# Optimization experiments

Measured on AMD Instinct MI355X. Metric: run time of the kernel, lower is better.

Reference implementation:

```python
import jax, jax.numpy as jnp
import numpy as np

N_NODES = 100000
N_EDGES = 3200000
NFEAT, NHID, NCLASS = 512, 256, 64


def spmm(rows, cols, vals, x):
    # out[i] = sum_{e: rows[e]==i} vals[e] * x[cols[e]]
    msgs = vals[:, None] * x[cols]  # [E, F]
    return jax.ops.segment_sum(msgs, rows, num_segments=N_NODES)


def setup_inputs() -> dict:
    key = jax.random.key(0)
    ks = jax.random.split(key, 12)
    x = jax.random.normal(ks[0], (N_NODES, NFEAT), dtype=jnp.float32)
    adj_rows = jax.random.randint(ks[1], (N_EDGES,), 0, N_NODES, dtype=jnp.int32)
    adj_cols = jax.random.randint(ks[2], (N_EDGES,), 0, N_NODES, dtype=jnp.int32)
    adj_vals = jax.random.uniform(ks[3], (N_EDGES,), dtype=jnp.float32)
    # xavier-uniform style init for linear weights
    def xavier(k, fan_in, fan_out):
        a = np.sqrt(6.0 / (fan_in + fan_out)).astype(np.float32)
        return jax.random.uniform(k, (fan_in, fan_out), minval=-a, maxval=a, dtype=jnp.float32)
    W1 = xavier(ks[4], NFEAT, NHID)
    b1 = jnp.zeros((NHID,), dtype=jnp.float32)
    W2 = xavier(ks[5], NHID, NCLASS)
    b2 = jnp.zeros((NCLASS,), dtype=jnp.float32)
    Wres = xavier(ks[6], NHID, NCLASS)
    bres = jnp.zeros((NCLASS,), dtype=jnp.float32)
    return {"x": x, "adj_rows": adj_rows, "adj_cols": adj_cols, "adj_vals": adj_vals,
            "W1": W1, "b1": b1, "W2": W2, "b2": b2, "Wres": Wres, "bres": bres}


def reference(x, adj_rows, adj_cols, adj_vals, W1, b1, W2, b2, Wres, bres):
    # layer 1: spmm -> linear (res_con True but last_hidden is None -> no residual)
    h = spmm(adj_rows, adj_cols, adj_vals, x)          # [N, NFEAT]
    h = h @ W1 + b1                                    # [N, NHID]
    last_hidden = h
    # dropout in eval mode: identity
    # layer 2: spmm -> linear -> relu + res(last_hidden) since NHID != NCLASS
    o = spmm(adj_rows, adj_cols, adj_vals, h)          # [N, NHID]
    o = o @ W2 + b2                                    # [N, NCLASS]
    o = jax.nn.relu(o) + (last_hidden @ Wres + bres)   # [N, NCLASS]
    return o
```

## Files before the change

### kernel.cpp

```cpp
#include <hip/hip_runtime.h>

#define N_NODES 100000
#define N_EDGES 3200000
#define NFEAT 512
#define NHID 256
#define NCLASS 64
#define FCAT 128

#define RPB 32
#define NB 3125
#define CHUNK 16384
#define NCH 196

#define ISC14 (1.0f / 16384.0f)
#define ISC10 (1.0f / 1024.0f)

typedef __attribute__((ext_vector_type(8))) short short8;
typedef __attribute__((ext_vector_type(4))) float f32x4;

static __device__ __forceinline__ unsigned short f2bf(float f) {
    unsigned u = __float_as_uint(f);
    unsigned r = (u + 0x7FFF + ((u >> 16) & 1)) >> 16;
    return (unsigned short)r;
}
static __device__ __forceinline__ short8 cvt8(float4 x, float4 y) {
    short8 r;
    r[0] = (short)f2bf(x.x); r[1] = (short)f2bf(x.y);
    r[2] = (short)f2bf(x.z); r[3] = (short)f2bf(x.w);
    r[4] = (short)f2bf(y.x); r[5] = (short)f2bf(y.y);
    r[6] = (short)f2bf(y.z); r[7] = (short)f2bf(y.w);
    return r;
}
__device__ __forceinline__ void gload_lds16(const unsigned short* g, unsigned short* l) {
    __builtin_amdgcn_global_load_lds(
        (const __attribute__((address_space(1))) unsigned int*)g,
        (__attribute__((address_space(3))) unsigned int*)l, 16, 0, 0);
}
static __device__ __forceinline__ int f2q4(float a) {
    return __float2int_rn(fminf(fmaxf(a, -7.9375f), 7.9375f) * 16.f);
}

__global__ __launch_bounds__(256) void k_fusedA(const float* __restrict__ W1,
                                                const float* __restrict__ W2,
                                                const float* __restrict__ Wres,
                                                const float* __restrict__ b1,
                                                const float* __restrict__ bres,
                                                unsigned short* __restrict__ WT,
                                                float* __restrict__ c2,
                                                float* __restrict__ cr,
                                                const int* __restrict__ rows,
                                                int* __restrict__ HT) {
    __shared__ int h[NB];
    int tid = threadIdx.x;
    if (blockIdx.x < 256) {
        int k = blockIdx.x * 2 + (tid >> 7);
        int j = tid & 127;
        const float* wb = (j < NCLASS) ? W2 : Wres;
        int jj = j & (NCLASS - 1);
        const float* w1row = W1 + (size_t)k * NHID;
        float acc = 0.f;
        for (int m = 0; m < NHID; ++m)
            acc += w1row[m] * wb[(size_t)m * NCLASS + jj];
        WT[(size_t)j * NFEAT + k] = f2bf(acc);
        return;
    }
    if (blockIdx.x == 256) {
        if (tid < 128) {
            int j = tid;
            const float* wb = (j < NCLASS) ? W2 : Wres;
            int jj = j & (NCLASS - 1);
            float acc = 0.f;
            for (int m = 0; m < NHID; ++m)
                acc += b1[m] * wb[(size_t)m * NCLASS + jj];
            if (j < NCLASS) c2[jj] = acc;
            else            cr[jj] = acc + bres[jj];
        }
        return;
    }
    int c = blockIdx.x - 257;
    for (int i = tid; i < NB; i += 256) h[i] = 0;
    __syncthreads();
    int e0 = c * CHUNK;
    int eend = e0 + CHUNK; if (eend > N_EDGES) eend = N_EDGES;
    int i = e0 + tid;
    for (; i + 7 * 256 < eend; i += 8 * 256) {
        int r[8];
#pragma unroll
        for (int u = 0; u < 8; ++u) r[u] = rows[i + u * 256];
#pragma unroll
        for (int u = 0; u < 8; ++u) atomicAdd(&h[r[u] >> 5], 1);
    }
    for (; i < eend; i += 256)
        atomicAdd(&h[rows[i] >> 5], 1);
    __syncthreads();
    for (int k = tid; k < NB; k += 256)
        HT[(size_t)k * NCH + c] = h[k];
}

__global__ void k_scan_chunks(const int* __restrict__ HT, int* __restrict__ OFS,
                              int* __restrict__ T) {
    int b = blockIdx.x;
    int lane = threadIdx.x;
    const int* hb = HT + (size_t)b * NCH;
    int run = 0;
    for (int c0 = 0; c0 < NCH; c0 += 64) {
        int idx = c0 + lane;
        int v = (idx < NCH) ? hb[idx] : 0;
        int inc = v;
#pragma unroll
        for (int d = 1; d < 64; d <<= 1) {
            int t = __shfl_up(inc, d);
            if (lane >= d) inc += t;
        }
        if (idx < NCH) OFS[(size_t)idx * NB + b] = run + inc - v;
        run += __shfl(inc, 63);
    }
    if (lane == 0) T[b] = run;
}

__global__ void k_scan_base(const int* __restrict__ T, int* __restrict__ base) {
    int lane = threadIdx.x;
    int run = 0;
    for (int c0 = 0; c0 < NB; c0 += 64) {
        int idx = c0 + lane;
        int v = (idx < NB) ? T[idx] : 0;
        int inc = v;
#pragma unroll
        for (int d = 1; d < 64; d <<= 1) {
            int t = __shfl_up(inc, d);
            if (lane >= d) inc += t;
        }
        if (idx < NB) base[idx] = run + inc - v;
        run += __shfl(inc, 63);
    }
    if (lane == 0) base[NB] = run;
}

__global__ __launch_bounds__(256) void k_partition(const int* __restrict__ rows,
                                                   const int* __restrict__ cols,
                                                   const float* __restrict__ vals,
                                                   const int* __restrict__ OFS,
                                                   const int* __restrict__ base,
                                                   unsigned* __restrict__ stage) {
    __shared__ int cur[NB];
    int c = blockIdx.x;
    int tid = threadIdx.x;
    for (int i = tid; i < NB; i += 256)
        cur[i] = base[i] + OFS[(size_t)c * NB + i];
    __syncthreads();
    int e0 = c * CHUNK;
    int eend = e0 + CHUNK; if (eend > N_EDGES) eend = N_EDGES;
    int i = e0 + tid;
    for (; i + 7 * 256 < eend; i += 8 * 256) {
        int r[8], cc[8]; float v[8];
#pragma unroll
        for (int u = 0; u < 8; ++u) r[u] = rows[i + u * 256];
#pragma unroll
        for (int u = 0; u < 8; ++u) cc[u] = cols[i + u * 256];
#pragma unroll
        for (int u = 0; u < 8; ++u) v[u] = vals[i + u * 256];
        int p[8];
#pragma unroll
        for (int u = 0; u < 8; ++u) p[u] = atomicAdd(&cur[r[u] >> 5], 1);
#pragma unroll
        for (int u = 0; u < 8; ++u) {
            unsigned v10 = min(1023u, (unsigned)__float2int_rn(v[u] * 1024.f));
            stage[p[u]] = (((unsigned)(r[u] & 31)) << 27) |
                          (((unsigned)cc[u]) << 10) | v10;
        }
    }
    for (; i < eend; i += 256) {
        int r = rows[i];
        int p = atomicAdd(&cur[r >> 5], 1);
        unsigned v10 = min(1023u, (unsigned)__float2int_rn(vals[i] * 1024.f));
        stage[p] = (((unsigned)(r & 31)) << 27) | (((unsigned)cols[i]) << 10) | v10;
    }
}

#define GBK 64
__global__ __launch_bounds__(256) void k_gemm_a(const float* __restrict__ X,
                                                const unsigned short* __restrict__ WT,
                                                unsigned short* __restrict__ A2) {
    __shared__ __align__(16) unsigned short Bs[2][FCAT * GBK];
    int tid = threadIdx.x;
    int lane = tid & 63, w = tid >> 6;
    int lr = lane & 15, ls = lane >> 4;
    int row = blockIdx.x * 64 + w * 16 + lr;
    if (row >= N_NODES) row = N_NODES - 1;
    const float* pA = X + (size_t)row * NFEAT;

#define STAGE(buf, k0)                                                         \
    {                                                                          \
        _Pragma("unroll")                                                      \
        for (int q = 0; q < 4; ++q) {                                          \
            int sidx = q * 256 + tid;                                          \
            int n = sidx >> 3, c8 = sidx & 7;                                  \
            const unsigned short* src =                                        \
                WT + (size_t)n * NFEAT + (k0) + ((c8 ^ (n & 7)) << 3);         \
            unsigned short* dst = &Bs[buf][(size_t)(q * 256 + w * 64) * 8];    \
            gload_lds16(src, dst);                                             \
        }                                                                      \
    }

    f32x4 acc[8] = {};
    STAGE(0, 0);
    float4 a00 = *(const float4*)(pA + ls * 8);
    float4 a01 = *(const float4*)(pA + ls * 8 + 4);
    float4 a10 = *(const float4*)(pA + 32 + ls * 8);
    float4 a11 = *(const float4*)(pA + 32 + ls * 8 + 4);
    __syncthreads();
    int cur = 0;

#pragma unroll
    for (int t = 0; t < 8; ++t) {
        float4 n00, n01, n10, n11;
        if (t < 7) {
            const int k1 = (t + 1) * GBK;
            n00 = *(const float4*)(pA + k1 + ls * 8);
            n01 = *(const float4*)(pA + k1 + ls * 8 + 4);
            n10 = *(const float4*)(pA + k1 + 32 + ls * 8);
            n11 = *(const float4*)(pA + k1 + 32 + ls * 8 + 4);
            STAGE(cur ^ 1, k1);
        }

        short8 af0 = cvt8(a00, a01);
        short8 af1 = cvt8(a10, a11);
        const unsigned short* bb = &Bs[cur][0];
#pragma unroll
        for (int nf = 0; nf < 8; ++nf) {
            int n = nf * 16 + lr;
            int p0 = ls ^ (n & 7);
            int p1 = (4 + ls) ^ (n & 7);
            short8 b0 = *(const short8*)(bb + (size_t)n * 64 + p0 * 8);
            short8 b1 = *(const short8*)(bb + (size_t)n * 64 + p1 * 8);
            acc[nf] = __builtin_amdgcn_mfma_f32_16x16x32_bf16(af0, b0, acc[nf], 0, 0, 0);
            acc[nf] = __builtin_amdgcn_mfma_f32_16x16x32_bf16(af1, b1, acc[nf], 0, 0, 0);
        }
        __syncthreads();
        cur ^= 1;
        a00 = n00; a01 = n01; a10 = n10; a11 = n11;
    }
#undef STAGE

#pragma unroll
    for (int j = 0; j < 4; ++j) {
        int gr = blockIdx.x * 64 + w * 16 + ls * 4 + j;
        if (gr < N_NODES) {
#pragma unroll
            for (int nf = 0; nf < 4; ++nf) {
                int il = f2q4(acc[nf][j]);
                int ih = f2q4(acc[nf + 4][j]);
                A2[(size_t)gr * 64 + nf * 16 + lr] =
                    (unsigned short)(((unsigned)il & 0xffu) | (((unsigned)ih & 0xffu) << 8));
            }
        }
    }
}

__global__ __launch_bounds__(256) void k_spmm1(const unsigned short* __restrict__ A2,
                                               const int* __restrict__ base,
                                               const unsigned* __restrict__ stage,
                                               unsigned short* __restrict__ S1a,
                                               float* __restrict__ S1r) {
    __shared__ int acc[RPB][FCAT];
    int b = blockIdx.x, tid = threadIdx.x;
    int wv = tid >> 6, lane = tid & 63;
    unsigned lane2 = (unsigned)lane << 1;
    int4* az = (int4*)&acc[0][0];
    for (int i = tid; i < RPB * FCAT / 4; i += 256) az[i] = make_int4(0, 0, 0, 0);
    __syncthreads();

    const char* A2b = (const char*)A2;

    int s = base[b], e = base[b + 1];
    int per = (e - s + 3) >> 2;
    int ws = s + wv * per;
    int we = ws + per; if (we > e) we = e;
    int t = ws;
    for (; t + 16 <= we; t += 16) {
        unsigned cv[16];
#pragma unroll
        for (int u = 0; u < 16; ++u) cv[u] = stage[t + u];
        unsigned short p[16];
#pragma unroll
        for (int u = 0; u < 16; ++u)
            p[u] = *(const unsigned short*)(A2b + (((cv[u] & 0x07FFFC00u) >> 3) | lane2));
#pragma unroll
        for (int u = 0; u < 16; ++u) {
            int v10 = (int)(cv[u] & 0x3FFu);
            int alo = (int)(signed char)(p[u] & 0xffu);
            int ahi = (int)(signed char)(p[u] >> 8);
            int rl = (int)(cv[u] >> 27);
            atomicAdd(&acc[rl][lane],      __mul24(alo, v10));
            atomicAdd(&acc[rl][lane + 64], __mul24(ahi, v10));
        }
    }
    for (; t < we; ++t) {
        unsigned cv = stage[t];
        unsigned short p = *(const unsigned short*)(A2b + (((cv & 0x07FFFC00u) >> 3) | lane2));
        int v10 = (int)(cv & 0x3FFu);
        int alo = (int)(signed char)(p & 0xffu);
        int ahi = (int)(signed char)(p >> 8);
        int rl = (int)(cv >> 27);
        atomicAdd(&acc[rl][lane],      __mul24(alo, v10));
        atomicAdd(&acc[rl][lane + 64], __mul24(ahi, v10));
    }
    __syncthreads();

#pragma unroll
    for (int rr = 0; rr < 8; ++rr) {
        int r = wv * 8 + rr;
        int node = b * RPB + r;
        int sf = (acc[r][lane] + 32) >> 6;
        sf = max(-32760, min(32760, sf));
        S1a[(size_t)node * 64 + (lane & 31) * 2 + (lane >> 5)] = (unsigned short)sf;
        S1r[(size_t)node * 64 + lane] = (float)acc[r][lane + 64] * ISC14;
    }
}

__global__ __launch_bounds__(256) void k_spmm2_out(const unsigned* __restrict__ S1aP,
                                                   const float* __restrict__ S1r,
                                                   const int* __restrict__ base,
                                                   const unsigned* __restrict__ stage,
                                                   const float* __restrict__ c2,
                                                   const float* __restrict__ cr,
                                                   const float* __restrict__ b2,
                                                   float* __restrict__ out) {
    __shared__ int acc[RPB][NCLASS];
    __shared__ int rs[RPB];
    int b = blockIdx.x, tid = threadIdx.x;
    int wv = tid >> 6, lane = tid & 63;
    int h = lane >> 5, l5 = lane & 31;
    unsigned l54 = (unsigned)l5 << 2;
    int4* az = (int4*)&acc[0][0];
    for (int i = tid; i < RPB * NCLASS / 4; i += 256) az[i] = make_int4(0, 0, 0, 0);
    if (tid < RPB) rs[tid] = 0;
    __syncthreads();

    const char* Sb = (const char*)S1aP;

    int s = base[b], e = base[b + 1];
    int per = (e - s + 3) >> 2;
    int ws = s + wv * per;
    int we = ws + per; if (we > e) we = e;
    int t = ws;
    for (; t + 32 <= we; t += 32) {
        unsigned cv[16];
#pragma unroll
        for (int u = 0; u < 16; ++u) cv[u] = stage[t + u * 2 + h];
        unsigned p[16];
#pragma unroll
        for (int u = 0; u < 16; ++u)
            p[u] = *(const unsigned*)(Sb + (((cv[u] & 0x07FFFC00u) >> 3) | l54));
#pragma unroll
        for (int u = 0; u < 16; ++u) {
            int v10 = (int)(cv[u] & 0x3FFu);
            int slo = (int)(short)(p[u] & 0xffffu);
            int shi = (int)p[u] >> 16;
            int rl = (int)(cv[u] >> 27);
            atomicAdd(&acc[rl][l5],      (__mul24(slo, v10) + 8) >> 4);
            atomicAdd(&acc[rl][l5 + 32], (__mul24(shi, v10) + 8) >> 4);
            if (l5 == 0) atomicAdd(&rs[rl], v10);
        }
    }
    for (; t < we; t += 2) {
        int idx = t + h;
        bool act = idx < we;
        unsigned cv = stage[act ? idx : t];
        unsigned p = *(const unsigned*)(Sb + (((cv & 0x07FFFC00u) >> 3) | l54));
        int v10 = (int)(cv & 0x3FFu);
        int slo = (int)(short)(p & 0xffffu);
        int shi = (int)p >> 16;
        int rl = (int)(cv >> 27);
        if (act) {
            atomicAdd(&acc[rl][l5],      (__mul24(slo, v10) + 8) >> 4);
            atomicAdd(&acc[rl][l5 + 32], (__mul24(shi, v10) + 8) >> 4);
            if (l5 == 0) atomicAdd(&rs[rl], v10);
        }
    }
    __syncthreads();

#pragma unroll
    for (int rr = 0; rr < 8; ++rr) {
        int r = wv * 8 + rr;
        int node = b * RPB + r;
        float facc = (float)acc[r][lane] * ISC14;
        float rsum = (float)rs[r] * ISC10;
        float o = facc + rsum * c2[lane] + b2[lane];
        float res = S1r[(size_t)node * 64 + lane] + cr[lane];
        out[(size_t)node * 64 + lane] = fmaxf(o, 0.f) + res;
    }
}

extern "C" void kernel_launch(void* const* d_in, const int* in_sizes, int n_in,
                              void* d_out, int out_size, void* d_ws, size_t ws_size,
                              hipStream_t stream) {
    const float* x        = (const float*)d_in[0];
    const int*   adj_rows = (const int*)d_in[1];
    const int*   adj_cols = (const int*)d_in[2];
    const float* adj_vals = (const float*)d_in[3];
    const float* W1       = (const float*)d_in[4];
    const float* b1       = (const float*)d_in[5];
    const float* W2       = (const float*)d_in[6];
    const float* b2       = (const float*)d_in[7];
    const float* Wres     = (const float*)d_in[8];
    const float* bres     = (const float*)d_in[9];
    float* out = (float*)d_out;

    char* ws = (char*)d_ws;
    size_t off = 0;
    auto alloc = [&](size_t bytes) {
        size_t o = off;
        off += (bytes + 511) & ~511ULL;
        return o;
    };

    unsigned short* WT  = (unsigned short*)(ws + alloc((size_t)NFEAT * FCAT * 2));
    float* c2           = (float*)(ws + alloc(NCLASS * 4));
    float* cr           = (float*)(ws + alloc(NCLASS * 4));
    unsigned* stage     = (unsigned*)(ws + alloc((size_t)N_EDGES * 4));
    unsigned short* A2  = (unsigned short*)(ws + alloc((size_t)N_NODES * 64 * 2));
    unsigned* S1a       = (unsigned*)(ws + alloc((size_t)N_NODES * 32 * 4));
    char* s1r_region    = ws + alloc((size_t)N_NODES * 64 * 4);
    float* S1r          = (float*)s1r_region;
    int*   HT           = (int*)s1r_region;
    int*   OFS          = (int*)(s1r_region + (((size_t)NB * NCH * 4 + 511) & ~511ULL));
    int*   T            = (int*)(ws + alloc((size_t)NB * 4));
    int*   base         = (int*)(ws + alloc((size_t)(NB + 1) * 4));
    (void)ws_size; (void)in_sizes; (void)n_in; (void)out_size;

    k_fusedA<<<257 + NCH, 256, 0, stream>>>(W1, W2, Wres, b1, bres, WT, c2, cr,
                                            adj_rows, HT);

    k_scan_chunks<<<NB, 64, 0, stream>>>(HT, OFS, T);
    k_scan_base<<<1, 64, 0, stream>>>(T, base);

    k_partition<<<NCH, 256, 0, stream>>>(adj_rows, adj_cols, adj_vals, OFS, base, stage);

    k_gemm_a<<<(N_NODES + 63) / 64, 256, 0, stream>>>(x, WT, A2);

    k_spmm1<<<NB, 256, 0, stream>>>(A2, base, stage, (unsigned short*)S1a, S1r);

    k_spmm2_out<<<NB, 256, 0, stream>>>(S1a, S1r, base, stage, c2, cr, b2, out);
}
```

Measured before the change: 310.3 us.

## Bucket edges by column tile within row blocks to improve gather locality

The counting-sort partition now keys each edge on both its row block and its column range, using four column tiles of 32768 nodes. Each SpMM block then walks the tiles in turn, so gathers from the feature arrays stay inside a narrower address window at any moment and should hit L2 more often. In exchange the histogram and offset tables become four times larger, the chunk count drops to 49 so the partition kernels have fewer blocks, and k_scan_base serially scans 12500 keys in a single wave. There are also more short segments per block, which adds loop overhead.

```diff
diff --git a/kernel.cpp b/kernel.cpp
--- a/kernel.cpp
+++ b/kernel.cpp
@@ -9,8 +9,10 @@
 
 #define RPB 32
 #define NB 3125
-#define CHUNK 16384
-#define NCH 196
+#define NCT 4
+#define NKEY (NCT * NB)
+#define CHUNK 65536
+#define NCH 49
 
 #define ISC14 (1.0f / 16384.0f)
 #define ISC10 (1.0f / 1024.0f)
@@ -49,8 +51,9 @@
                                                 float* __restrict__ c2,
                                                 float* __restrict__ cr,
                                                 const int* __restrict__ rows,
+                                                const int* __restrict__ cols,
                                                 int* __restrict__ HT) {
-    __shared__ int h[NB];
+    __shared__ int h[NKEY];
     int tid = threadIdx.x;
     if (blockIdx.x < 256) {
         int k = blockIdx.x * 2 + (tid >> 7);
@@ -78,22 +81,25 @@
         return;
     }
     int c = blockIdx.x - 257;
-    for (int i = tid; i < NB; i += 256) h[i] = 0;
+    for (int i = tid; i < NKEY; i += 256) h[i] = 0;
     __syncthreads();
     int e0 = c * CHUNK;
     int eend = e0 + CHUNK; if (eend > N_EDGES) eend = N_EDGES;
     int i = e0 + tid;
     for (; i + 7 * 256 < eend; i += 8 * 256) {
-        int r[8];
+        int r[8], cc[8];
 #pragma unroll
         for (int u = 0; u < 8; ++u) r[u] = rows[i + u * 256];
 #pragma unroll
-        for (int u = 0; u < 8; ++u) atomicAdd(&h[r[u] >> 5], 1);
+        for (int u = 0; u < 8; ++u) cc[u] = cols[i + u * 256];
+#pragma unroll
+        for (int u = 0; u < 8; ++u)
+            atomicAdd(&h[(cc[u] >> 15) * NB + (r[u] >> 5)], 1);
     }
     for (; i < eend; i += 256)
-        atomicAdd(&h[rows[i] >> 5], 1);
-    __syncthreads();
-    for (int k = tid; k < NB; k += 256)
+        atomicAdd(&h[(cols[i] >> 15) * NB + (rows[i] >> 5)], 1);
+    __syncthreads();
+    for (int k = tid; k < NKEY; k += 256)
         HT[(size_t)k * NCH + c] = h[k];
 }
 
@@ -112,41 +118,41 @@
             int t = __shfl_up(inc, d);
             if (lane >= d) inc += t;
         }
-        if (idx < NCH) OFS[(size_t)idx * NB + b] = run + inc - v;
+        if (idx < NCH) OFS[(size_t)idx * NKEY + b] = run + inc - v;
         run += __shfl(inc, 63);
     }
     if (lane == 0) T[b] = run;
 }
 
-__global__ void k_scan_base(const int* __restrict__ T, int* __restrict__ base) {
+__global__ void k_scan_base(const int* __restrict__ T, int* __restrict__ base2) {
     int lane = threadIdx.x;
     int run = 0;
-    for (int c0 = 0; c0 < NB; c0 += 64) {
+    for (int c0 = 0; c0 < NKEY; c0 += 64) {
         int idx = c0 + lane;
-        int v = (idx < NB) ? T[idx] : 0;
+        int v = (idx < NKEY) ? T[idx] : 0;
         int inc = v;
 #pragma unroll
         for (int d = 1; d < 64; d <<= 1) {
             int t = __shfl_up(inc, d);
             if (lane >= d) inc += t;
         }
-        if (idx < NB) base[idx] = run + inc - v;
+        if (idx < NKEY) base2[idx] = run + inc - v;
         run += __shfl(inc, 63);
     }
-    if (lane == 0) base[NB] = run;
+    if (lane == 0) base2[NKEY] = run;
 }
 
 __global__ __launch_bounds__(256) void k_partition(const int* __restrict__ rows,
                                                    const int* __restrict__ cols,
                                                    const float* __restrict__ vals,
                                                    const int* __restrict__ OFS,
-                                                   const int* __restrict__ base,
+                                                   const int* __restrict__ base2,
                                                    unsigned* __restrict__ stage) {
-    __shared__ int cur[NB];
+    __shared__ int cur[NKEY];
     int c = blockIdx.x;
     int tid = threadIdx.x;
-    for (int i = tid; i < NB; i += 256)
-        cur[i] = base[i] + OFS[(size_t)c * NB + i];
+    for (int i = tid; i < NKEY; i += 256)
+        cur[i] = base2[i] + OFS[(size_t)c * NKEY + i];
     __syncthreads();
     int e0 = c * CHUNK;
     int eend = e0 + CHUNK; if (eend > N_EDGES) eend = N_EDGES;
@@ -161,7 +167,8 @@
         for (int u = 0; u < 8; ++u) v[u] = vals[i + u * 256];
         int p[8];
 #pragma unroll
-        for (int u = 0; u < 8; ++u) p[u] = atomicAdd(&cur[r[u] >> 5], 1);
+        for (int u = 0; u < 8; ++u)
+            p[u] = atomicAdd(&cur[(cc[u] >> 15) * NB + (r[u] >> 5)], 1);
 #pragma unroll
         for (int u = 0; u < 8; ++u) {
             unsigned v10 = min(1023u, (unsigned)__float2int_rn(v[u] * 1024.f));
@@ -170,10 +177,10 @@
         }
     }
     for (; i < eend; i += 256) {
-        int r = rows[i];
-        int p = atomicAdd(&cur[r >> 5], 1);
+        int r = rows[i], cc = cols[i];
+        int p = atomicAdd(&cur[(cc >> 15) * NB + (r >> 5)], 1);
         unsigned v10 = min(1023u, (unsigned)__float2int_rn(vals[i] * 1024.f));
-        stage[p] = (((unsigned)(r & 31)) << 27) | (((unsigned)cols[i]) << 10) | v10;
+        stage[p] = (((unsigned)(r & 31)) << 27) | (((unsigned)cc) << 10) | v10;
     }
 }
 
@@ -258,7 +265,7 @@
 }
 
 __global__ __launch_bounds__(256) void k_spmm1(const unsigned short* __restrict__ A2,
-                                               const int* __restrict__ base,
+                                               const int* __restrict__ base2,
                                                const unsigned* __restrict__ stage,
                                                unsigned short* __restrict__ S1a,
                                                float* __restrict__ S1r) {
@@ -272,38 +279,40 @@
 
     const char* A2b = (const char*)A2;
 
-    int s = base[b], e = base[b + 1];
-    int per = (e - s + 3) >> 2;
-    int ws = s + wv * per;
-    int we = ws + per; if (we > e) we = e;
-    int t = ws;
-    for (; t + 16 <= we; t += 16) {
-        unsigned cv[16];
-#pragma unroll
-        for (int u = 0; u < 16; ++u) cv[u] = stage[t + u];
-        unsigned short p[16];
-#pragma unroll
-        for (int u = 0; u < 16; ++u)
-            p[u] = *(const unsigned short*)(A2b + (((cv[u] & 0x07FFFC00u) >> 3) | lane2));
-#pragma unroll
-        for (int u = 0; u < 16; ++u) {
-            int v10 = (int)(cv[u] & 0x3FFu);
-            int alo = (int)(signed char)(p[u] & 0xffu);
-            int ahi = (int)(signed char)(p[u] >> 8);
-            int rl = (int)(cv[u] >> 27);
+    for (int ct = 0; ct < NCT; ++ct) {
+        int s = base2[ct * NB + b], e = base2[ct * NB + b + 1];
+        int per = (e - s + 3) >> 2;
+        int ws = s + wv * per;
+        int we = ws + per; if (we > e) we = e;
+        int t = ws;
+        for (; t + 16 <= we; t += 16) {
+            unsigned cv[16];
+#pragma unroll
+            for (int u = 0; u < 16; ++u) cv[u] = stage[t + u];
+            unsigned short p[16];
+#pragma unroll
+            for (int u = 0; u < 16; ++u)
+                p[u] = *(const unsigned short*)(A2b + (((cv[u] & 0x07FFFC00u) >> 3) | lane2));
+#pragma unroll
+            for (int u = 0; u < 16; ++u) {
+                int v10 = (int)(cv[u] & 0x3FFu);
+                int alo = (int)(signed char)(p[u] & 0xffu);
+                int ahi = (int)(signed char)(p[u] >> 8);
+                int rl = (int)(cv[u] >> 27);
+                atomicAdd(&acc[rl][lane],      __mul24(alo, v10));
+                atomicAdd(&acc[rl][lane + 64], __mul24(ahi, v10));
+            }
+        }
+        for (; t < we; ++t) {
+            unsigned cv = stage[t];
+            unsigned short p = *(const unsigned short*)(A2b + (((cv & 0x07FFFC00u) >> 3) | lane2));
+            int v10 = (int)(cv & 0x3FFu);
+            int alo = (int)(signed char)(p & 0xffu);
+            int ahi = (int)(signed char)(p >> 8);
+            int rl = (int)(cv >> 27);
             atomicAdd(&acc[rl][lane],      __mul24(alo, v10));
             atomicAdd(&acc[rl][lane + 64], __mul24(ahi, v10));
         }
-    }
-    for (; t < we; ++t) {
-        unsigned cv = stage[t];
-        unsigned short p = *(const unsigned short*)(A2b + (((cv & 0x07FFFC00u) >> 3) | lane2));
-        int v10 = (int)(cv & 0x3FFu);
-        int alo = (int)(signed char)(p & 0xffu);
-        int ahi = (int)(signed char)(p >> 8);
-        int rl = (int)(cv >> 27);
-        atomicAdd(&acc[rl][lane],      __mul24(alo, v10));
-        atomicAdd(&acc[rl][lane + 64], __mul24(ahi, v10));
     }
     __syncthreads();
 
@@ -320,7 +329,7 @@
 
 __global__ __launch_bounds__(256) void k_spmm2_out(const unsigned* __restrict__ S1aP,
                                                    const float* __restrict__ S1r,
-                                                   const int* __restrict__ base,
+                                                   const int* __restrict__ base2,
                                                    const unsigned* __restrict__ stage,
                                                    const float* __restrict__ c2,
                                                    const float* __restrict__ cr,
@@ -339,43 +348,45 @@
 
     const char* Sb = (const char*)S1aP;
 
-    int s = base[b], e = base[b + 1];
-    int per = (e - s + 3) >> 2;
-    int ws = s + wv * per;
-    int we = ws + per; if (we > e) we = e;
-    int t = ws;
-    for (; t + 32 <= we; t += 32) {
-        unsigned cv[16];
-#pragma unroll
-        for (int u = 0; u < 16; ++u) cv[u] = stage[t + u * 2 + h];
-        unsigned p[16];
-#pragma unroll
-        for (int u = 0; u < 16; ++u)
-            p[u] = *(const unsigned*)(Sb + (((cv[u] & 0x07FFFC00u) >> 3) | l54));
-#pragma unroll
-        for (int u = 0; u < 16; ++u) {
-            int v10 = (int)(cv[u] & 0x3FFu);
-            int slo = (int)(short)(p[u] & 0xffffu);
-            int shi = (int)p[u] >> 16;
-            int rl = (int)(cv[u] >> 27);
-            atomicAdd(&acc[rl][l5],      (__mul24(slo, v10) + 8) >> 4);
-            atomicAdd(&acc[rl][l5 + 32], (__mul24(shi, v10) + 8) >> 4);
-            if (l5 == 0) atomicAdd(&rs[rl], v10);
-        }
-    }
-    for (; t < we; t += 2) {
-        int idx = t + h;
-        bool act = idx < we;
-        unsigned cv = stage[act ? idx : t];
-        unsigned p = *(const unsigned*)(Sb + (((cv & 0x07FFFC00u) >> 3) | l54));
-        int v10 = (int)(cv & 0x3FFu);
-        int slo = (int)(short)(p & 0xffffu);
-        int shi = (int)p >> 16;
-        int rl = (int)(cv >> 27);
-        if (act) {
-            atomicAdd(&acc[rl][l5],      (__mul24(slo, v10) + 8) >> 4);
-            atomicAdd(&acc[rl][l5 + 32], (__mul24(shi, v10) + 8) >> 4);
-            if (l5 == 0) atomicAdd(&rs[rl], v10);
+    for (int ct = 0; ct < NCT; ++ct) {
+        int s = base2[ct * NB + b], e = base2[ct * NB + b + 1];
+        int per = (e - s + 3) >> 2;
+        int ws = s + wv * per;
+        int we = ws + per; if (we > e) we = e;
+        int t = ws;
+        for (; t + 32 <= we; t += 32) {
+            unsigned cv[16];
+#pragma unroll
+            for (int u = 0; u < 16; ++u) cv[u] = stage[t + u * 2 + h];
+            unsigned p[16];
+#pragma unroll
+            for (int u = 0; u < 16; ++u)
+                p[u] = *(const unsigned*)(Sb + (((cv[u] & 0x07FFFC00u) >> 3) | l54));
+#pragma unroll
+            for (int u = 0; u < 16; ++u) {
+                int v10 = (int)(cv[u] & 0x3FFu);
+                int slo = (int)(short)(p[u] & 0xffffu);
+                int shi = (int)p[u] >> 16;
+                int rl = (int)(cv[u] >> 27);
+                atomicAdd(&acc[rl][l5],      (__mul24(slo, v10) + 8) >> 4);
+                atomicAdd(&acc[rl][l5 + 32], (__mul24(shi, v10) + 8) >> 4);
+                if (l5 == 0) atomicAdd(&rs[rl], v10);
+            }
+        }
+        for (; t < we; t += 2) {
+            int idx = t + h;
+            bool act = idx < we;
+            unsigned cv = stage[act ? idx : t];
+            unsigned p = *(const unsigned*)(Sb + (((cv & 0x07FFFC00u) >> 3) | l54));
+            int v10 = (int)(cv & 0x3FFu);
+            int slo = (int)(short)(p & 0xffffu);
+            int shi = (int)p >> 16;
+            int rl = (int)(cv >> 27);
+            if (act) {
+                atomicAdd(&acc[rl][l5],      (__mul24(slo, v10) + 8) >> 4);
+                atomicAdd(&acc[rl][l5 + 32], (__mul24(shi, v10) + 8) >> 4);
+                if (l5 == 0) atomicAdd(&rs[rl], v10);
+            }
         }
     }
     __syncthreads();
@@ -424,22 +435,22 @@
     char* s1r_region    = ws + alloc((size_t)N_NODES * 64 * 4);
     float* S1r          = (float*)s1r_region;
     int*   HT           = (int*)s1r_region;
-    int*   OFS          = (int*)(s1r_region + (((size_t)NB * NCH * 4 + 511) & ~511ULL));
-    int*   T            = (int*)(ws + alloc((size_t)NB * 4));
-    int*   base         = (int*)(ws + alloc((size_t)(NB + 1) * 4));
+    int*   OFS          = (int*)(s1r_region + (((size_t)NKEY * NCH * 4 + 511) & ~511ULL));
+    int*   T            = (int*)(ws + alloc((size_t)NKEY * 4));
+    int*   base2        = (int*)(ws + alloc((size_t)(NKEY + 1) * 4));
     (void)ws_size; (void)in_sizes; (void)n_in; (void)out_size;
 
     k_fusedA<<<257 + NCH, 256, 0, stream>>>(W1, W2, Wres, b1, bres, WT, c2, cr,
-                                            adj_rows, HT);
-
-    k_scan_chunks<<<NB, 64, 0, stream>>>(HT, OFS, T);
-    k_scan_base<<<1, 64, 0, stream>>>(T, base);
-
-    k_partition<<<NCH, 256, 0, stream>>>(adj_rows, adj_cols, adj_vals, OFS, base, stage);
+                                            adj_rows, adj_cols, HT);
+
+    k_scan_chunks<<<NKEY, 64, 0, stream>>>(HT, OFS, T);
+    k_scan_base<<<1, 64, 0, stream>>>(T, base2);
+
+    k_partition<<<NCH, 256, 0, stream>>>(adj_rows, adj_cols, adj_vals, OFS, base2, stage);
 
     k_gemm_a<<<(N_NODES + 63) / 64, 256, 0, stream>>>(x, WT, A2);
 
-    k_spmm1<<<NB, 256, 0, stream>>>(A2, base, stage, (unsigned short*)S1a, S1r);
-
-    k_spmm2_out<<<NB, 256, 0, stream>>>(S1a, S1r, base, stage, c2, cr, b2, out);
-}
+    k_spmm1<<<NB, 256, 0, stream>>>(A2, base2, stage, (unsigned short*)S1a, S1r);
+
+    k_spmm2_out<<<NB, 256, 0, stream>>>(S1a, S1r, base2, stage, c2, cr, b2, out);
+}
```

After: 491.5 us. 1.58x slower.
